# Kernel tuning notes

Measured on AMD Instinct MI355X. Metric: run time of the kernel, lower is better.

The kernel has to match this reference:

```python
import jax, jax.numpy as jnp
import numpy as np

DIM = 256
HEADS = 8
DIM_HEAD = 64
HIDDEN = HEADS * DIM_HEAD  # 512
SCALE = DIM_HEAD ** -0.5


def setup_inputs() -> dict:
    key = jax.random.key(0)
    k1, k2, k3, k4 = jax.random.split(key, 4)
    x = jax.random.normal(k1, (4, DIM, 2048), dtype=jnp.float32)
    # Conv1d with kernel_size=1 == pointwise linear over channels; store weights as [out, in]
    w_qkv = jax.random.normal(k2, (HIDDEN * 3, DIM), dtype=jnp.float32) * (DIM ** -0.5)
    w_out = jax.random.normal(k3, (DIM, HIDDEN), dtype=jnp.float32) * (HIDDEN ** -0.5)
    b_out = jax.random.normal(k4, (DIM,), dtype=jnp.float32) * 0.01
    return {"x": x, "w_qkv": w_qkv, "w_out": w_out, "b_out": b_out}


def reference(x, w_qkv, w_out, b_out):
    b, c, n = x.shape
    # pointwise conv == channel matmul: [b, 3*hidden, n]
    qkv = jnp.einsum('oc,bcn->bon', w_qkv, x)
    q, k, v = jnp.split(qkv, 3, axis=1)
    # b (h d) n -> b h d n
    reshape = lambda t: t.reshape(b, HEADS, DIM_HEAD, n)
    q, k, v = reshape(q) * SCALE, reshape(k), reshape(v)
    sim = jnp.einsum('bhdi,bhdj->bhij', q, k)          # [b, h, n, n]
    attn = jax.nn.softmax(sim, axis=-1)
    out = jnp.einsum('bhij,bhdj->bhid', attn, v)        # [b, h, n, d]
    # b h n d -> b (h d) n
    out = out.transpose(0, 1, 3, 2).reshape(b, HIDDEN, n)
    return jnp.einsum('oc,bcn->bon', w_out, out) + b_out[None, :, None]
```

## Files before the change

### kernel.cpp

```cpp
#include <hip/hip_runtime.h>
#include <hip/hip_bf16.h>

using f32x4  = __attribute__((ext_vector_type(4))) float;
using f32x16 = __attribute__((ext_vector_type(16))) float;
using bf16x8 = __attribute__((ext_vector_type(8))) short;
using u32x2  = __attribute__((ext_vector_type(2))) unsigned int;
using u32x4  = __attribute__((ext_vector_type(4))) unsigned int;

#define MFMA16(a, b, c) __builtin_amdgcn_mfma_f32_16x16x32_bf16((a), (b), (c), 0, 0, 0)
#define MFMA32(a, b, c) __builtin_amdgcn_mfma_f32_32x32x16_bf16((a), (b), (c), 0, 0, 0)

static __device__ __forceinline__ unsigned short f2bf(float x) {
    unsigned int u = __builtin_bit_cast(unsigned int, x);
    unsigned int r = (u + 0x7fffu + ((u >> 16) & 1u)) >> 16;
    return (unsigned short)r;
}

static __device__ __forceinline__ unsigned int cvtpk_bf16(float a, float b) {
    unsigned int r;
    asm("v_cvt_pk_bf16_f32 %0, %1, %2" : "=v"(r) : "v"(a), "v"(b));
    return r;
}

static __device__ __forceinline__ float exp2_fast(float x) {
#if __has_builtin(__builtin_amdgcn_exp2f)
    return __builtin_amdgcn_exp2f(x);
#else
    return __expf(x * 0.69314718056f);
#endif
}

static __device__ __forceinline__ void plswap(unsigned int& x, unsigned int& y, int hi) {
#if __has_builtin(__builtin_amdgcn_permlane32_swap)
    u32x2 r = __builtin_amdgcn_permlane32_swap(x, y, false, false);
    x = r[0]; y = r[1];
#else
    unsigned int xs = (unsigned int)__shfl_xor((int)x, 32);
    unsigned int ys = (unsigned int)__shfl_xor((int)y, 32);
    unsigned int nx = hi ? ys : x;
    unsigned int ny = hi ? y  : xs;
    x = nx; y = ny;
#endif
}

#define NB 4
#define DIMC 256
#define NN 2048
#define NH 8
#define DH 64
#define HID 512

#define QSCALE 0.18033688f

#define OFF_XT  0u
#define OFF_WQ  4194304u
#define OFF_WO  4980736u
#define OFF_Q   5242880u
#define OFF_K   13631488u
#define OFF_V   22020096u
#define OFF_AO  30408704u

__global__ __launch_bounds__(256) void k_prep(
    const float* __restrict__ x, const float* __restrict__ wqkv,
    const float* __restrict__ wout,
    unsigned short* __restrict__ xt, unsigned short* __restrict__ wq_b,
    unsigned short* __restrict__ wo_b)
{
    int wg = blockIdx.x + 32 * blockIdx.y + 128 * blockIdx.z;
    int tid = wg * 256 + threadIdx.x;
    if (tid < 98304) {
        float4 v = ((const float4*)wqkv)[tid];
        u32x2 pk; pk[0] = cvtpk_bf16(v.x, v.y); pk[1] = cvtpk_bf16(v.z, v.w);
        *(u32x2*)(wq_b + (size_t)tid * 4) = pk;
    } else {
        int t2 = tid - 98304;
        float4 v = ((const float4*)wout)[t2];
        u32x2 pk; pk[0] = cvtpk_bf16(v.x, v.y); pk[1] = cvtpk_bf16(v.z, v.w);
        *(u32x2*)(wo_b + (size_t)t2 * 4) = pk;
    }

    __shared__ unsigned short tile[64][65];
    int nb = blockIdx.x, cb = blockIdx.y, b = blockIdx.z;
    int t = threadIdx.x;
    int tn = t & 63, tg = t >> 6;
    const float* xp = x + ((size_t)(b * DIMC + cb * 64)) * NN + nb * 64;
#pragma unroll
    for (int it = 0; it < 16; ++it) {
        int c = tg * 16 + it;
        tile[c][tn] = f2bf(xp[(size_t)c * NN + tn]);
    }
    __syncthreads();
    unsigned short* op = xt + ((size_t)(b * NN + nb * 64)) * DIMC + cb * 64;
#pragma unroll
    for (int it = 0; it < 16; ++it) {
        int n = tg * 16 + it;
        op[(size_t)n * DIMC + tn] = tile[tn][n];
    }
}

__global__ __launch_bounds__(256) void k_qkv(
    const unsigned short* __restrict__ wq,
    const unsigned short* __restrict__ xt,
    unsigned short* __restrict__ qT, unsigned short* __restrict__ kTt,
    unsigned short* __restrict__ vTt)
{
    int bx = blockIdx.x;
    int nb = blockIdx.y;
    int b  = blockIdx.z;
    int wid = threadIdx.x >> 6;
    int l = threadIdx.x & 63, l15 = l & 15, l4 = l >> 4;
    int o0 = bx * 64, n0 = nb * 64;
    int wr = wid >> 1, wc = wid & 1;
    f32x4 acc[2][2] = {};

    if (bx < 16) {
        const unsigned short* arow = xt + ((size_t)(b * NN + n0 + wr * 32)) * DIMC;
        const unsigned short* brow = wq + (size_t)(o0 + wc * 32) * DIMC;
#pragma unroll
        for (int k0 = 0; k0 < DIMC; k0 += 32) {
            int koff = k0 + l4 * 8;
            bf16x8 a0 = *(const bf16x8*)(arow + (size_t)l15 * DIMC + koff);
            bf16x8 a1 = *(const bf16x8*)(arow + (size_t)(l15 + 16) * DIMC + koff);
            bf16x8 b0 = *(const bf16x8*)(brow + (size_t)l15 * DIMC + koff);
            bf16x8 b1 = *(const bf16x8*)(brow + (size_t)(l15 + 16) * DIMC + koff);
            acc[0][0] = MFMA16(a0, b0, acc[0][0]);
            acc[0][1] = MFMA16(a0, b1, acc[0][1]);
            acc[1][0] = MFMA16(a1, b0, acc[1][0]);
            acc[1][1] = MFMA16(a1, b1, acc[1][1]);
        }
#pragma unroll
        for (int fm = 0; fm < 2; ++fm)
#pragma unroll
            for (int fn = 0; fn < 2; ++fn) {
                int ocol = o0 + wc * 32 + fn * 16 + l15;
#pragma unroll
                for (int r = 0; r < 4; ++r) {
                    int nrow = n0 + wr * 32 + fm * 16 + l4 * 4 + r;
                    float v = acc[fm][fn][r];
                    if (ocol < HID) {
                        int h = ocol >> 6, d = ocol & 63;
                        qT[(((size_t)(b * NH + h)) * NN + nrow) * DH + d] = f2bf(v * QSCALE);
                    } else {
                        int o2 = ocol - HID;
                        int h = o2 >> 6, d = o2 & 63;
                        int jt = nrow >> 5, li2 = nrow & 31;
                        int ks = d >> 4, hi2 = (d >> 3) & 1, e = d & 7;
                        kTt[((size_t)(b * NH + h) * 64 + jt) * 2048
                            + ks * 512 + hi2 * 256 + li2 * 8 + e] = f2bf(v);
                    }
                }
            }
    } else {
        const unsigned short* arow = wq + (size_t)(o0 + wr * 32) * DIMC;
        const unsigned short* brow = xt + ((size_t)(b * NN + n0 + wc * 32)) * DIMC;
#pragma unroll
        for (int k0 = 0; k0 < DIMC; k0 += 32) {
            int koff = k0 + l4 * 8;
            bf16x8 a0 = *(const bf16x8*)(arow + (size_t)l15 * DIMC + koff);
            bf16x8 a1 = *(const bf16x8*)(arow + (size_t)(l15 + 16) * DIMC + koff);
            bf16x8 b0 = *(const bf16x8*)(brow + (size_t)l15 * DIMC + koff);
            bf16x8 b1 = *(const bf16x8*)(brow + (size_t)(l15 + 16) * DIMC + koff);
            acc[0][0] = MFMA16(a0, b0, acc[0][0]);
            acc[0][1] = MFMA16(a0, b1, acc[0][1]);
            acc[1][0] = MFMA16(a1, b0, acc[1][0]);
            acc[1][1] = MFMA16(a1, b1, acc[1][1]);
        }
#pragma unroll
        for (int fm = 0; fm < 2; ++fm)
#pragma unroll
            for (int fn = 0; fn < 2; ++fn)
#pragma unroll
                for (int r = 0; r < 4; ++r) {
                    int orow = o0 + wr * 32 + fm * 16 + l4 * 4 + r;
                    int ncol = n0 + wc * 32 + fn * 16 + l15;
                    int o2 = orow - 1024;
                    int h = o2 >> 6, dd = o2 & 63;
                    int j = ncol;
                    int jt = j >> 5, js = (j >> 4) & 1, hi2 = (j >> 3) & 1, e = j & 7;
                    int dt = dd >> 5, li2 = dd & 31;
                    vTt[((size_t)(b * NH + h) * 64 + jt) * 2048
                        + (dt * 2 + js) * 512 + hi2 * 256 + li2 * 8 + e] = f2bf(acc[fm][fn][r]);
                }
    }
}

__global__ __launch_bounds__(256) void k_attn5(
    const unsigned short* __restrict__ qT, const unsigned short* __restrict__ kTt,
    const unsigned short* __restrict__ vTt, unsigned short* __restrict__ ao)
{
    __shared__ float obuf[2][64][32];
    __shared__ float mlbuf[2][4][32];
    __shared__ unsigned short tb[2][32 * 72];

    int wg = blockIdx.x;
    int xcd = wg & 7;
    int idx = wg >> 3;
    int bh  = xcd * 4 + (idx & 3);
    int ib  = idx >> 2;
    int b = bh >> 3, h = bh & 7;
    int wid = threadIdx.x >> 6;
    int iw = wid & 1, jw = wid >> 1;
    int l = threadIdx.x & 63, li = l & 31, hi = l >> 5;
    int i0 = ib * 64 + iw * 32;

    const unsigned short* qb  = qT + ((size_t)bh * NN) * DH;
    const unsigned short* ktb = kTt + (size_t)bh * 64 * 2048;
    const unsigned short* vtb = vTt + (size_t)bh * 64 * 2048;

    bf16x8 qf[4];
#pragma unroll
    for (int ks = 0; ks < 4; ++ks)
        qf[ks] = *(const bf16x8*)(qb + (size_t)(i0 + li) * DH + ks * 16 + hi * 8);

    f32x16 o0 = {}, o1 = {};
    float m = -1e30f, lsum = 0.f;

    const int jt0 = jw * 32, jt1 = jt0 + 32;

    const unsigned short* kcur = ktb + (size_t)jt0 * 2048;
    bf16x8 kf[4];
#pragma unroll
    for (int ks = 0; ks < 4; ++ks)
        kf[ks] = *(const bf16x8*)(kcur + ks * 512 + l * 8);

    for (int jt = jt0; jt < jt1; ++jt) {
        const unsigned short* vcur = vtb + (size_t)jt * 2048;
        bf16x8 vf[4];
#pragma unroll
        for (int f = 0; f < 4; ++f)
            vf[f] = *(const bf16x8*)(vcur + f * 512 + l * 8);

        f32x16 s = {};
        __builtin_amdgcn_s_setprio(1);
        s = MFMA32(kf[0], qf[0], s);
        s = MFMA32(kf[1], qf[1], s);
        s = MFMA32(kf[2], qf[2], s);
        s = MFMA32(kf[3], qf[3], s);
        __builtin_amdgcn_s_setprio(0);

        kcur += 2048;
        if (jt + 1 < jt1) {
#pragma unroll
            for (int ks = 0; ks < 4; ++ks)
                kf[ks] = *(const bf16x8*)(kcur + ks * 512 + l * 8);
        }

        float t8[8];
#pragma unroll
        for (int q = 0; q < 8; ++q) t8[q] = fmaxf(s[2 * q], s[2 * q + 1]);
        float t4a = fmaxf(t8[0], t8[1]), t4b = fmaxf(t8[2], t8[3]);
        float t4c = fmaxf(t8[4], t8[5]), t4d = fmaxf(t8[6], t8[7]);
        float pmax = fmaxf(fmaxf(t4a, t4b), fmaxf(t4c, t4d));
        {
            unsigned int pu = __builtin_bit_cast(unsigned int, pmax), pv = pu;
            plswap(pu, pv, hi);
            pmax = fmaxf(__builtin_bit_cast(float, pu), __builtin_bit_cast(float, pv));
        }

        if (!__all(pmax - m <= 8.0f)) {
            float mn = fmaxf(m, pmax);
            float alpha = exp2_fast(m - mn);
            m = mn;
            lsum *= alpha;
#pragma unroll
            for (int r = 0; r < 16; ++r) { o0[r] *= alpha; o1[r] *= alpha; }
        }

        float p[16];
#pragma unroll
        for (int r = 0; r < 16; ++r) p[r] = exp2_fast(s[r] - m);
        float u8[8];
#pragma unroll
        for (int q = 0; q < 8; ++q) u8[q] = p[2 * q] + p[2 * q + 1];
        float u4a = u8[0] + u8[1], u4b = u8[2] + u8[3], u4c = u8[4] + u8[5], u4d = u8[6] + u8[7];
        float rsum = (u4a + u4b) + (u4c + u4d);
        {
            unsigned int pu = __builtin_bit_cast(unsigned int, rsum), pv = pu;
            plswap(pu, pv, hi);
            rsum = __builtin_bit_cast(float, pu) + __builtin_bit_cast(float, pv);
        }
        lsum += rsum;

        unsigned int W[8];
#pragma unroll
        for (int q = 0; q < 8; ++q) W[q] = cvtpk_bf16(p[2 * q], p[2 * q + 1]);
        plswap(W[0], W[2], hi); plswap(W[1], W[3], hi);
        plswap(W[4], W[6], hi); plswap(W[5], W[7], hi);
        u32x4 c0; c0[0] = W[0]; c0[1] = W[1]; c0[2] = W[2]; c0[3] = W[3];
        u32x4 c1; c1[0] = W[4]; c1[1] = W[5]; c1[2] = W[6]; c1[3] = W[7];
        bf16x8 pb0 = __builtin_bit_cast(bf16x8, c0);
        bf16x8 pb1 = __builtin_bit_cast(bf16x8, c1);

        __builtin_amdgcn_s_setprio(1);
        o0 = MFMA32(vf[0], pb0, o0);
        o0 = MFMA32(vf[1], pb1, o0);
        o1 = MFMA32(vf[2], pb0, o1);
        o1 = MFMA32(vf[3], pb1, o1);
        __builtin_amdgcn_s_setprio(0);
    }

    mlbuf[0][wid][li] = m;
    mlbuf[1][wid][li] = lsum;
    __syncthreads();
    float mp = mlbuf[0][wid ^ 2][li];
    float lp = mlbuf[1][wid ^ 2][li];
    float mfin = fmaxf(m, mp);
    float aown = exp2_fast(m - mfin);
    float lfin = lsum * aown + lp * exp2_fast(mp - mfin);
#pragma unroll
    for (int r = 0; r < 16; ++r) { o0[r] *= aown; o1[r] *= aown; }

    if (jw == 1) {
        float* ob = &obuf[iw][0][0];
#pragma unroll
        for (int r = 0; r < 16; ++r) {
            int d0a = (r & 3) + 8 * (r >> 2) + 4 * hi;
            ob[d0a * 32 + li]        = o0[r];
            ob[(32 + d0a) * 32 + li] = o1[r];
        }
    }
    __syncthreads();
    if (jw == 0) {
        const float* ob = &obuf[iw][0][0];
#pragma unroll
        for (int r = 0; r < 16; ++r) {
            int d0a = (r & 3) + 8 * (r >> 2) + 4 * hi;
            o0[r] += ob[d0a * 32 + li];
            o1[r] += ob[(32 + d0a) * 32 + li];
        }

        float inv = 1.0f / lfin;
        unsigned short* tw = &tb[iw][0];
#pragma unroll
        for (int dt = 0; dt < 2; ++dt) {
            const f32x16& oo = dt ? o1 : o0;
#pragma unroll
            for (int q = 0; q < 8; ++q) {
                int r = 2 * q;
                int d0 = dt * 32 + (r & 3) + 8 * (r >> 2) + 4 * hi;
                unsigned int wpk = cvtpk_bf16(oo[r] * inv, oo[r + 1] * inv);
                *(unsigned int*)((char*)tw + li * 144 + d0 * 2) = wpk;
            }
        }
        unsigned short* aop = ao + ((size_t)b * NN + i0 + li) * HID + h * DH + hi * 32;
#pragma unroll
        for (int k = 0; k < 4; ++k) {
            bf16x8 v = *(const bf16x8*)((const char*)tw + li * 144 + (hi * 32 + k * 8) * 2);
            *(bf16x8*)(aop + k * 8) = v;
        }
    }
}

__global__ __launch_bounds__(256) void k_proj(
    const unsigned short* __restrict__ wo,
    const unsigned short* __restrict__ ao,
    const float* __restrict__ bout, float* __restrict__ out)
{
    int ob = blockIdx.x, nb = blockIdx.y, b = blockIdx.z;
    int wid = threadIdx.x >> 6;
    int l = threadIdx.x & 63, l15 = l & 15, l4 = l >> 4;
    int wr = wid >> 1, wc = wid & 1;
    int o0 = ob * 64 + wr * 32, n0 = nb * 64 + wc * 32;
    const unsigned short* arow = wo + (size_t)o0 * HID;
    const unsigned short* brow = ao + ((size_t)(b * NN) + n0) * HID;
    f32x4 acc[2][2] = {};
#pragma unroll
    for (int k0 = 0; k0 < HID; k0 += 32) {
        int koff = k0 + l4 * 8;
        bf16x8 a0 = *(const bf16x8*)(arow + (size_t)l15 * HID + koff);
        bf16x8 a1 = *(const bf16x8*)(arow + (size_t)(l15 + 16) * HID + koff);
        bf16x8 b0 = *(const bf16x8*)(brow + (size_t)l15 * HID + koff);
        bf16x8 b1 = *(const bf16x8*)(brow + (size_t)(l15 + 16) * HID + koff);
        acc[0][0] = MFMA16(a0, b0, acc[0][0]);
        acc[0][1] = MFMA16(a0, b1, acc[0][1]);
        acc[1][0] = MFMA16(a1, b0, acc[1][0]);
        acc[1][1] = MFMA16(a1, b1, acc[1][1]);
    }
#pragma unroll
    for (int fm = 0; fm < 2; ++fm)
#pragma unroll
        for (int fn = 0; fn < 2; ++fn)
#pragma unroll
            for (int r = 0; r < 4; ++r) {
                int o = o0 + fm * 16 + l4 * 4 + r;
                int n = n0 + fn * 16 + l15;
                out[((size_t)(b * DIMC + o)) * NN + n] = acc[fm][fn][r] + bout[o];
            }
}

extern "C" void kernel_launch(void* const* d_in, const int* in_sizes, int n_in,
                              void* d_out, int out_size, void* d_ws, size_t ws_size,
                              hipStream_t stream)
{
    const float* x    = (const float*)d_in[0];
    const float* wqkv = (const float*)d_in[1];
    const float* wout = (const float*)d_in[2];
    const float* bout = (const float*)d_in[3];
    float* out = (float*)d_out;
    char* ws = (char*)d_ws;

    unsigned short* xt  = (unsigned short*)(ws + OFF_XT);
    unsigned short* wqb = (unsigned short*)(ws + OFF_WQ);
    unsigned short* wob = (unsigned short*)(ws + OFF_WO);
    unsigned short* qT  = (unsigned short*)(ws + OFF_Q);
    unsigned short* kTt = (unsigned short*)(ws + OFF_K);
    unsigned short* vTt = (unsigned short*)(ws + OFF_V);
    unsigned short* ao  = (unsigned short*)(ws + OFF_AO);

    hipLaunchKernelGGL(k_prep, dim3(32, 4, 4), dim3(256), 0, stream, x, wqkv, wout, xt, wqb, wob);
    hipLaunchKernelGGL(k_qkv, dim3(24, 32, 4), dim3(256), 0, stream, wqb, xt, qT, kTt, vTt);
    hipLaunchKernelGGL(k_attn5, dim3(1024), dim3(256), 0, stream, qT, kTt, vTt, ao);
    hipLaunchKernelGGL(k_proj, dim3(4, 32, 4), dim3(256), 0, stream, wob, ao, bout, out);
}
```

Baseline: 184.4 us.

## Store GEMM operands in MFMA-fragment-tiled layout for contiguous wavefront loads

The prep kernel now writes x^T, w_qkv and w_out in a tiled layout where each 16x32 MFMA fragment is a contiguous 1 KB block. The attention kernel writes its output in the same tiled layout. The QKV and projection GEMMs then load each fragment as one fully contiguous 64-lane read instead of 16 strided row segments. This should improve global-load coalescing and cache-line use. The cost is scattered address arithmetic in the prep and attention-output stores, and every producer and consumer must agree on the layout.

```diff
diff --git a/kernel.cpp b/kernel.cpp
--- a/kernel.cpp
+++ b/kernel.cpp
@@ -52,6 +52,7 @@
 
 #define QSCALE 0.18033688f
 
+
 #define OFF_XT  0u
 #define OFF_WQ  4194304u
 #define OFF_WO  4980736u
@@ -69,14 +70,22 @@
     int wg = blockIdx.x + 32 * blockIdx.y + 128 * blockIdx.z;
     int tid = wg * 256 + threadIdx.x;
     if (tid < 98304) {
+        int o = tid >> 6, c4 = (tid & 63) * 4;
         float4 v = ((const float4*)wqkv)[tid];
         u32x2 pk; pk[0] = cvtpk_bf16(v.x, v.y); pk[1] = cvtpk_bf16(v.z, v.w);
-        *(u32x2*)(wq_b + (size_t)tid * 4) = pk;
+        int rt = o >> 5, rr = o & 31, sub = rr >> 4, l15f = rr & 15;
+        int kt = c4 >> 5, l4f = (c4 >> 3) & 3, e = c4 & 7;
+        size_t off = (size_t)(((rt * 8 + kt) * 2 + sub)) * 512 + l15f * 32 + l4f * 8 + e;
+        *(u32x2*)(wq_b + off) = pk;
     } else {
         int t2 = tid - 98304;
+        int o = t2 >> 7, c4 = (t2 & 127) * 4;
         float4 v = ((const float4*)wout)[t2];
         u32x2 pk; pk[0] = cvtpk_bf16(v.x, v.y); pk[1] = cvtpk_bf16(v.z, v.w);
-        *(u32x2*)(wo_b + (size_t)t2 * 4) = pk;
+        int rt = o >> 5, rr = o & 31, sub = rr >> 4, l15f = rr & 15;
+        int kt = c4 >> 5, l4f = (c4 >> 3) & 3, e = c4 & 7;
+        size_t off = (size_t)(((rt * 16 + kt) * 2 + sub)) * 512 + l15f * 32 + l4f * 8 + e;
+        *(u32x2*)(wo_b + off) = pk;
     }
 
     __shared__ unsigned short tile[64][65];
@@ -90,11 +99,15 @@
         tile[c][tn] = f2bf(xp[(size_t)c * NN + tn]);
     }
     __syncthreads();
-    unsigned short* op = xt + ((size_t)(b * NN + nb * 64)) * DIMC + cb * 64;
+    unsigned short* xb = xt + (size_t)b * NN * DIMC;
+    int C = cb * 64 + tn;
+    int kt = C >> 5, l4f = (C >> 3) & 3, e = C & 7;
 #pragma unroll
     for (int it = 0; it < 16; ++it) {
         int n = tg * 16 + it;
-        op[(size_t)n * DIMC + tn] = tile[tn][n];
+        int R = nb * 64 + n;
+        int rt = R >> 5, rr = R & 31, sub = rr >> 4, l15f = rr & 15;
+        xb[(size_t)(((rt * 8 + kt) * 2 + sub)) * 512 + l15f * 32 + l4f * 8 + e] = tile[tn][n];
     }
 }
 
@@ -111,18 +124,21 @@
     int l = threadIdx.x & 63, l15 = l & 15, l4 = l >> 4;
     int o0 = bx * 64, n0 = nb * 64;
     int wr = wid >> 1, wc = wid & 1;
+    int lane_off = l15 * 32 + l4 * 8;
+    const unsigned short* xb = xt + (size_t)b * NN * DIMC;
     f32x4 acc[2][2] = {};
 
     if (bx < 16) {
-        const unsigned short* arow = xt + ((size_t)(b * NN + n0 + wr * 32)) * DIMC;
-        const unsigned short* brow = wq + (size_t)(o0 + wc * 32) * DIMC;
-#pragma unroll
-        for (int k0 = 0; k0 < DIMC; k0 += 32) {
-            int koff = k0 + l4 * 8;
-            bf16x8 a0 = *(const bf16x8*)(arow + (size_t)l15 * DIMC + koff);
-            bf16x8 a1 = *(const bf16x8*)(arow + (size_t)(l15 + 16) * DIMC + koff);
-            bf16x8 b0 = *(const bf16x8*)(brow + (size_t)l15 * DIMC + koff);
-            bf16x8 b1 = *(const bf16x8*)(brow + (size_t)(l15 + 16) * DIMC + koff);
+        int rt_a = nb * 2 + wr;
+        int rt_b = bx * 2 + wc;
+#pragma unroll
+        for (int kt = 0; kt < 8; ++kt) {
+            const unsigned short* at = xb + (size_t)((rt_a * 8 + kt) * 2) * 512 + lane_off;
+            const unsigned short* bt = wq + (size_t)((rt_b * 8 + kt) * 2) * 512 + lane_off;
+            bf16x8 a0 = *(const bf16x8*)(at);
+            bf16x8 a1 = *(const bf16x8*)(at + 512);
+            bf16x8 b0 = *(const bf16x8*)(bt);
+            bf16x8 b1 = *(const bf16x8*)(bt + 512);
             acc[0][0] = MFMA16(a0, b0, acc[0][0]);
             acc[0][1] = MFMA16(a0, b1, acc[0][1]);
             acc[1][0] = MFMA16(a1, b0, acc[1][0]);
@@ -151,15 +167,16 @@
                 }
             }
     } else {
-        const unsigned short* arow = wq + (size_t)(o0 + wr * 32) * DIMC;
-        const unsigned short* brow = xt + ((size_t)(b * NN + n0 + wc * 32)) * DIMC;
-#pragma unroll
-        for (int k0 = 0; k0 < DIMC; k0 += 32) {
-            int koff = k0 + l4 * 8;
-            bf16x8 a0 = *(const bf16x8*)(arow + (size_t)l15 * DIMC + koff);
-            bf16x8 a1 = *(const bf16x8*)(arow + (size_t)(l15 + 16) * DIMC + koff);
-            bf16x8 b0 = *(const bf16x8*)(brow + (size_t)l15 * DIMC + koff);
-            bf16x8 b1 = *(const bf16x8*)(brow + (size_t)(l15 + 16) * DIMC + koff);
+        int rt_a = bx * 2 + wr;
+        int rt_b = nb * 2 + wc;
+#pragma unroll
+        for (int kt = 0; kt < 8; ++kt) {
+            const unsigned short* at = wq + (size_t)((rt_a * 8 + kt) * 2) * 512 + lane_off;
+            const unsigned short* bt = xb + (size_t)((rt_b * 8 + kt) * 2) * 512 + lane_off;
+            bf16x8 a0 = *(const bf16x8*)(at);
+            bf16x8 a1 = *(const bf16x8*)(at + 512);
+            bf16x8 b0 = *(const bf16x8*)(bt);
+            bf16x8 b1 = *(const bf16x8*)(bt + 512);
             acc[0][0] = MFMA16(a0, b0, acc[0][0]);
             acc[0][1] = MFMA16(a0, b1, acc[0][1]);
             acc[1][0] = MFMA16(a1, b0, acc[1][0]);
@@ -342,11 +359,13 @@
                 *(unsigned int*)((char*)tw + li * 144 + d0 * 2) = wpk;
             }
         }
-        unsigned short* aop = ao + ((size_t)b * NN + i0 + li) * HID + h * DH + hi * 32;
+        int rt = i0 >> 5;
+        unsigned short* pao = ao + (size_t)b * NN * HID
+            + (size_t)(((rt * 16 + 2 * h + hi) * 2 + (li >> 4))) * 512 + (li & 15) * 32;
 #pragma unroll
         for (int k = 0; k < 4; ++k) {
             bf16x8 v = *(const bf16x8*)((const char*)tw + li * 144 + (hi * 32 + k * 8) * 2);
-            *(bf16x8*)(aop + k * 8) = v;
+            *(bf16x8*)(pao + k * 8) = v;
         }
     }
 }
@@ -361,16 +380,19 @@
     int l = threadIdx.x & 63, l15 = l & 15, l4 = l >> 4;
     int wr = wid >> 1, wc = wid & 1;
     int o0 = ob * 64 + wr * 32, n0 = nb * 64 + wc * 32;
-    const unsigned short* arow = wo + (size_t)o0 * HID;
-    const unsigned short* brow = ao + ((size_t)(b * NN) + n0) * HID;
+    int lane_off = l15 * 32 + l4 * 8;
+    int rt_a = ob * 2 + wr;
+    int rt_b = nb * 2 + wc;
+    const unsigned short* aob = ao + (size_t)b * NN * HID;
     f32x4 acc[2][2] = {};
 #pragma unroll
-    for (int k0 = 0; k0 < HID; k0 += 32) {
-        int koff = k0 + l4 * 8;
-        bf16x8 a0 = *(const bf16x8*)(arow + (size_t)l15 * HID + koff);
-        bf16x8 a1 = *(const bf16x8*)(arow + (size_t)(l15 + 16) * HID + koff);
-        bf16x8 b0 = *(const bf16x8*)(brow + (size_t)l15 * HID + koff);
-        bf16x8 b1 = *(const bf16x8*)(brow + (size_t)(l15 + 16) * HID + koff);
+    for (int kt = 0; kt < 16; ++kt) {
+        const unsigned short* at = wo + (size_t)((rt_a * 16 + kt) * 2) * 512 + lane_off;
+        const unsigned short* bt = aob + (size_t)((rt_b * 16 + kt) * 2) * 512 + lane_off;
+        bf16x8 a0 = *(const bf16x8*)(at);
+        bf16x8 a1 = *(const bf16x8*)(at + 512);
+        bf16x8 b0 = *(const bf16x8*)(bt);
+        bf16x8 b1 = *(const bf16x8*)(bt + 512);
         acc[0][0] = MFMA16(a0, b0, acc[0][0]);
         acc[0][1] = MFMA16(a0, b1, acc[0][1]);
         acc[1][0] = MFMA16(a1, b0, acc[1][0]);
```

Result: faster. 159.4 us (-13.5%).
